# Optimization experiments

Hardware: AMD Instinct MI355X
Metric: run time of the kernel (lower is better)

## Reference

```python
import jax, jax.numpy as jnp
import numpy as np

EMA_A = 0.4      # exponential moving average decay used in Hash_ExpMovAverage
WIN = 9          # window_size
LN_EPS = 1e-3    # keras LayerNormalization default epsilon


def setup_inputs() -> dict:
    key = jax.random.key(0)
    ks = jax.random.split(key, 8)
    B, N, D, H = 8, 4096, 256, 8
    w = lambda k, shape: jax.random.normal(k, shape, jnp.float32) * 0.05
    return {
        "x": jax.random.normal(ks[0], (B, N, D), jnp.float32),
        "head_kernel": w(ks[1], (D, H, D)),
        "head_bias": w(ks[2], (H, D)),
        "down_kernel": w(ks[3], (H, D, D)),
        "down_bias": w(ks[4], (D,)),
        "value_kernel": w(ks[5], (D, D)),
        "value_bias": w(ks[6], (D,)),
        "ln_gamma": jnp.ones((D,), jnp.float32),
        "ln_beta": jnp.zeros((D,), jnp.float32),
    }


def reference(x, head_kernel, head_bias, down_kernel, down_bias,
              value_kernel, value_bias, ln_gamma, ln_beta):
    B, N, D = x.shape
    half = (WIN - 1) // 2

    # Up_Projection: [B,N,D] -> [B,N,H,D], relu
    q = jax.nn.relu(jnp.einsum('bnd,dhe->bnhe', x, head_kernel) + head_bias)

    # ---- Neighborhoods_Arrangement ----
    # Neighborhood_SimHash: sign codes from relu activations, summed over heads
    codes = 2.0 * jnp.minimum(jnp.ceil(q), 1.0) - 1.0        # [B,N,H,D]
    lsh = jnp.sum(codes, axis=-2)                            # [B,N,D]
    # Hash_ExpMovAverage: sort descending along D, add positional encoding, EMA dot
    pos = jnp.argsort(-lsh, axis=-1)                         # descending order
    lsh_sorted = jnp.take_along_axis(lsh, pos, axis=-1)
    pf = pos.astype(jnp.float32)
    freq = 10.0 ** (-(pf / jnp.float32(D)))                  # 1 / 10**powers
    pe = jnp.sin(freq) * (pf % 2) + jnp.cos(freq) * (1.0 - pf % 2)
    vals = lsh_sorted + pe / EMA_A
    c = EMA_A * (1.0 - EMA_A) ** jnp.arange(D, dtype=jnp.float32)
    simv = jnp.einsum('bnd,d->bn', vals, c)                  # [B,N]
    order = jnp.argsort(simv, axis=-1)                       # ascending
    q = jnp.take_along_axis(q, order[:, :, None, None], axis=1)  # reorder tokens

    # Down_Projection: [B,N,H,D] -> [B,N,D], relu
    q = jax.nn.relu(jnp.einsum('bnhd,hde->bne', q, down_kernel) + down_bias)

    # (matches tile-first / extract_patches / tile-last concat in the original)
    starts = jnp.clip(jnp.arange(N) - half, 0, N - WIN)      # [N]
    widx = starts[:, None] + jnp.arange(WIN)[None, :]
    keyw = q[:, widx]

    scale = jnp.sqrt(jnp.float32(D))
    scores = jax.nn.softmax(jnp.einsum('bnd,bnwd->bnw', q, keyw) / scale, axis=-1)
    value = jax.nn.relu(jnp.einsum('bnwd,de->bnwe', keyw, value_kernel) + value_bias)
    attn_out = jnp.einsum('bnwd,bnw->bnd', value, scores)

    # Residual with ORIGINAL (un-permuted) inputs + LayerNorm (keras default eps)
    y = attn_out + x
    mu = jnp.mean(y, axis=-1, keepdims=True)
    var = jnp.var(y, axis=-1, keepdims=True)
    return (y - mu) / jnp.sqrt(var + LN_EPS) * ln_gamma + ln_beta
```

## Files before the change

kernel.cpp:

```cpp
#include <hip/hip_runtime.h>

constexpr int Bc = 8, Nc = 4096;
constexpr int TN = 16;
constexpr int TN3 = 32;
constexpr int XS3 = 36;

using short8 = __attribute__((ext_vector_type(8))) short;
using f32x4  = __attribute__((ext_vector_type(4))) float;

static __device__ __forceinline__ unsigned short f2bf(float f) {
    unsigned u = __float_as_uint(f);
    u += 0x7fffu + ((u >> 16) & 1u);
    return (unsigned short)(u >> 16);
}
static __device__ __forceinline__ int swz(int r, int k) {
    return (r << 9) + ((k << 1) ^ ((r & 7) << 4));
}

__global__ __launch_bounds__(256)
void k0_wdt(const float* __restrict__ Wd, unsigned short* __restrict__ WdT)
{
    __shared__ float tile[64][65];
    const int h  = blockIdx.x >> 4;
    const int t  = blockIdx.x & 15;
    const int kb = (t >> 2) * 64, eb = (t & 3) * 64;
    const int tid = threadIdx.x;
    {
        const int krow = tid >> 2, ec = (tid & 3) * 16;
        const float* src = Wd + h * 65536 + (kb + krow) * 256 + eb + ec;
        #pragma unroll
        for (int i = 0; i < 4; ++i) {
            float4 v = *reinterpret_cast<const float4*>(src + i * 4);
            tile[krow][ec + i * 4 + 0] = v.x;
            tile[krow][ec + i * 4 + 1] = v.y;
            tile[krow][ec + i * 4 + 2] = v.z;
            tile[krow][ec + i * 4 + 3] = v.w;
        }
    }
    __syncthreads();
    {
        const int erow = tid >> 2, dc = (tid & 3) * 16;
        unsigned short o[16];
        #pragma unroll
        for (int i = 0; i < 16; ++i) o[i] = f2bf(tile[dc + i][erow]);
        unsigned short* dst = WdT + h * 65536 + (eb + erow) * 256 + kb + dc;
        *reinterpret_cast<short8*>(dst)     = *reinterpret_cast<short8*>(&o[0]);
        *reinterpret_cast<short8*>(dst + 8) = *reinterpret_cast<short8*>(&o[8]);
    }
}

__global__ __launch_bounds__(256)
void k0_wht(const float* __restrict__ Wh, unsigned short* __restrict__ WhH,
            float* __restrict__ WhT)
{
    __shared__ float tile[64][65];
    const int h  = blockIdx.x >> 4;
    const int t  = blockIdx.x & 15;
    const int kb = (t >> 2) * 64, eb = (t & 3) * 64;
    const int tid = threadIdx.x;
    {
        const int krow = tid >> 2, ec = (tid & 3) * 16;
        const float* src = Wh + (kb + krow) * 2048 + h * 256 + eb + ec;
        #pragma unroll
        for (int i = 0; i < 4; ++i) {
            float4 v = *reinterpret_cast<const float4*>(src + i * 4);
            tile[krow][ec + i * 4 + 0] = v.x;
            tile[krow][ec + i * 4 + 1] = v.y;
            tile[krow][ec + i * 4 + 2] = v.z;
            tile[krow][ec + i * 4 + 3] = v.w;
        }
    }
    __syncthreads();
    {
        const int erow = tid >> 2, dc = (tid & 3) * 16;
        unsigned short o[16];
        float of[16];
        #pragma unroll
        for (int i = 0; i < 16; ++i) {
            of[i] = tile[dc + i][erow];
            o[i] = f2bf(of[i]);
        }
        const long base = (long)h * 65536 + (eb + erow) * 256 + kb + dc;
        *reinterpret_cast<short8*>(WhH + base)     = *reinterpret_cast<short8*>(&o[0]);
        *reinterpret_cast<short8*>(WhH + base + 8) = *reinterpret_cast<short8*>(&o[8]);
        #pragma unroll
        for (int i = 0; i < 16; i += 4)
            *reinterpret_cast<float4*>(WhT + base + i) = *reinterpret_cast<const float4*>(&of[i]);
    }
}

#define XSH_OFF 0
#define QTB_OFF 8192
#define LSH_OFF 16384
#define PE_OFF  32768
#define CF_OFF  33792
#define CNT_OFF 34816
#define FCN_OFF 35840
#define FLS_OFF 35856
#define FLS_CAP 1024
#define GUARD   0.012f

__global__ __launch_bounds__(256, 2)
void k1_head_down(const float* __restrict__ x,
                  const float* __restrict__ bh,
                  const float* __restrict__ WhT,
                  const unsigned short* __restrict__ WhH,
                  const unsigned short* __restrict__ WdT, const float* __restrict__ bd,
                  float* __restrict__ z, float* __restrict__ simv)
{
    __shared__ __align__(16) char SM[40192];

    const int tid = threadIdx.x;
    const long rowbase = (long)blockIdx.x * TN;
    const int wavei = tid >> 6, lane = tid & 63;
    const int mrow = lane & 15, kgrp = lane >> 4;
    const int ebase = wavei * 64 + mrow;
    const int kfo = kgrp * 8;

    {
        const int d = tid;
        const float u = -((float)d * 0.00390625f);
        const float freq = (float)pow(10.0, (double)u);
        const float pe = (d & 1) ? (float)sin((double)freq)
                                 : (float)cos((double)freq);
        ((float*)(SM + PE_OFF))[d] = __fdiv_rn(pe, 0.4f);
        ((float*)(SM + CF_OFF))[d] = __fmul_rn(0.4f, (float)pow((double)0.6f, (double)d));
    }
    if (tid == 0) *((int*)(SM + FCN_OFF)) = 0;
    {
        const int r = tid >> 4, kc = (tid & 15) * 16;
        const float* src = x + (rowbase + r) * 256 + kc;
        unsigned short oh[16];
        #pragma unroll
        for (int i = 0; i < 16; i += 4) {
            float4 v = *reinterpret_cast<const float4*>(src + i);
            oh[i + 0] = f2bf(v.x); oh[i + 1] = f2bf(v.y);
            oh[i + 2] = f2bf(v.z); oh[i + 3] = f2bf(v.w);
        }
        *reinterpret_cast<short8*>(SM + XSH_OFF + swz(r, kc))     = *reinterpret_cast<short8*>(&oh[0]);
        *reinterpret_cast<short8*>(SM + XSH_OFF + swz(r, kc + 8)) = *reinterpret_cast<short8*>(&oh[8]);
    }

    short8 hb[3][4], db[3][4];
    #pragma unroll
    for (int nf = 0; nf < 4; ++nf) {
        hb[0][nf] = *reinterpret_cast<const short8*>(&WhH[(ebase + nf * 16) * 256 + kfo]);
        hb[1][nf] = *reinterpret_cast<const short8*>(&WhH[(ebase + nf * 16) * 256 + 32 + kfo]);
    }

    unsigned lshp0 = 0, lshp1 = 0;
    f32x4 dacc[4];
    #pragma unroll
    for (int nf = 0; nf < 4; ++nf) dacc[nf] = (f32x4){0.f, 0.f, 0.f, 0.f};

    __syncthreads();

    for (int h = 0; h < 8; ++h) {
        const unsigned short* whh = WhH + ((long)h << 16);
        const unsigned short* wdh = WdT + ((long)h << 16);
        float bias[4];
        #pragma unroll
        for (int nf = 0; nf < 4; ++nf) bias[nf] = bh[(h << 8) + ebase + nf * 16];

        f32x4 hacc[4];
        #pragma unroll
        for (int nf = 0; nf < 4; ++nf) hacc[nf] = (f32x4){0.f, 0.f, 0.f, 0.f};
        #pragma unroll
        for (int kt = 0; kt < 8; ++kt) {
            const int k0 = kt * 32 + kfo;
            short8 afh = *reinterpret_cast<const short8*>(SM + XSH_OFF + swz(mrow, k0));
            if (kt < 6) {
                #pragma unroll
                for (int nf = 0; nf < 4; ++nf)
                    hb[(kt + 2) % 3][nf] = *reinterpret_cast<const short8*>(
                        &whh[(ebase + nf * 16) * 256 + k0 + 64]);
            }
            if (kt == 6) {
                #pragma unroll
                for (int nf = 0; nf < 4; ++nf)
                    db[0][nf] = *reinterpret_cast<const short8*>(
                        &wdh[(ebase + nf * 16) * 256 + kfo]);
            }
            if (kt == 7) {
                #pragma unroll
                for (int nf = 0; nf < 4; ++nf)
                    db[1][nf] = *reinterpret_cast<const short8*>(
                        &wdh[(ebase + nf * 16) * 256 + 32 + kfo]);
            }
            #pragma unroll
            for (int nf = 0; nf < 4; ++nf)
                hacc[nf] = __builtin_amdgcn_mfma_f32_16x16x32_bf16(afh, hb[kt % 3][nf], hacc[nf], 0, 0, 0);
        }
        #pragma unroll
        for (int nf = 0; nf < 4; ++nf) {
            const int e = ebase + nf * 16;
            #pragma unroll
            for (int reg = 0; reg < 4; ++reg) {
                const int r = kgrp * 4 + reg;
                const float pre = __fadd_rn(hacc[nf][reg], bias[nf]);
                const unsigned pos = (pre > 0.0f) ? 1u : 0u;
                const int j = nf * 4 + reg;
                if (j < 8) lshp0 += pos << (4 * j); else lshp1 += pos << (4 * (j - 8));
                if (fabsf(pre) < GUARD) {
                    int idx = atomicAdd((int*)(SM + FCN_OFF), 1);
                    if (idx < FLS_CAP)
                        ((int*)(SM + FLS_OFF))[idx] =
                            r | (e << 4) | (h << 12) | ((int)pos << 15);
                }
                *reinterpret_cast<unsigned short*>(SM + QTB_OFF + swz(r, e)) =
                    f2bf(fmaxf(pre, 0.0f));
            }
        }
        __syncthreads();
        #pragma unroll
        for (int ks = 0; ks < 8; ++ks) {
            const int k0 = ks * 32 + kfo;
            short8 af = *reinterpret_cast<const short8*>(SM + QTB_OFF + swz(mrow, k0));
            if (ks < 6) {
                #pragma unroll
                for (int nf = 0; nf < 4; ++nf)
                    db[(ks + 2) % 3][nf] = *reinterpret_cast<const short8*>(
                        &wdh[(ebase + nf * 16) * 256 + k0 + 64]);
            }
            if (ks == 6 && h < 7) {
                #pragma unroll
                for (int nf = 0; nf < 4; ++nf)
                    hb[0][nf] = *reinterpret_cast<const short8*>(
                        &WhH[((long)(h + 1) << 16) + (ebase + nf * 16) * 256 + kfo]);
            }
            if (ks == 7 && h < 7) {
                #pragma unroll
                for (int nf = 0; nf < 4; ++nf)
                    hb[1][nf] = *reinterpret_cast<const short8*>(
                        &WhH[((long)(h + 1) << 16) + (ebase + nf * 16) * 256 + 32 + kfo]);
            }
            #pragma unroll
            for (int nf = 0; nf < 4; ++nf)
                dacc[nf] = __builtin_amdgcn_mfma_f32_16x16x32_bf16(af, db[ks % 3][nf], dacc[nf], 0, 0, 0);
        }
        __syncthreads();
    }
    #pragma unroll
    for (int nf = 0; nf < 4; ++nf) {
        const int e = ebase + nf * 16;
        const float b = bd[e];
        #pragma unroll
        for (int reg = 0; reg < 4; ++reg) {
            const int m = kgrp * 4 + reg;
            z[(rowbase + m) * 256 + e] = fmaxf(dacc[nf][reg] + b, 0.0f);
        }
    }
    {
        int* lshI = (int*)(SM + LSH_OFF);
        #pragma unroll
        for (int nf = 0; nf < 4; ++nf) {
            const int e = ebase + nf * 16;
            #pragma unroll
            for (int reg = 0; reg < 4; ++reg) {
                const int j = nf * 4 + reg;
                const unsigned p = ((j < 8) ? (lshp0 >> (4 * j)) : (lshp1 >> (4 * (j - 8)))) & 15u;
                lshI[e * 16 + kgrp * 4 + reg] = 2 * (int)p - 8;
            }
        }
    }
    __syncthreads();
    {
        int n = *((int*)(SM + FCN_OFF));
        n = n < FLS_CAP ? n : FLS_CAP;
        for (int i = tid; i < n; i += 256) {
            const int ent = ((int*)(SM + FLS_OFF))[i];
            const int r = ent & 15, e = (ent >> 4) & 255, hh2 = (ent >> 12) & 7;
            const int fs = ((ent >> 15) & 1) ? 1 : -1;
            const float* xr = x + (rowbase + r) * 256;
            const float* wrow = WhT + (((long)hh2 << 8) + e) * 256;
            float acc = 0.0f;
            for (int k = 0; k < 256; k += 4) {
                float4 xv = *reinterpret_cast<const float4*>(xr + k);
                float4 wv = *reinterpret_cast<const float4*>(wrow + k);
                acc = fmaf(xv.x, wv.x, acc);
                acc = fmaf(xv.y, wv.y, acc);
                acc = fmaf(xv.z, wv.z, acc);
                acc = fmaf(xv.w, wv.w, acc);
            }
            const float pre = __fadd_rn(acc, bh[hh2 * 256 + e]);
            const int es = (pre > 0.0f) ? 1 : -1;
            if (es != fs)
                atomicAdd(&((int*)(SM + LSH_OFF))[e * 16 + r], es - fs);
        }
    }
    __syncthreads();
    if (tid < TN) {
        const int r = tid;
        const int* lshI = (const int*)(SM + LSH_OFF);
        const float* pe_over = (const float*)(SM + PE_OFF);
        const float* c_f = (const float*)(SM + CF_OFF);
        int* cw = (int*)(SM + CNT_OFF) + r * 16;
        for (int i = 0; i < 9; ++i) cw[i] = 0;
        for (int d = 0; d < 256; ++d) {
            int vv = lshI[d * 16 + r];
            cw[(vv + 8) >> 1] += 1;
        }
        int run = 0;
        for (int bin = 8; bin >= 0; --bin) { int c0 = cw[bin]; cw[bin] = run; run += c0; }
        float* valq = (float*)(SM + r * 1024);
        for (int d = 0; d < 256; ++d) {
            int vv = lshI[d * 16 + r];
            int bin = (vv + 8) >> 1;
            int j = cw[bin]++;
            valq[j] = __fadd_rn((float)vv, pe_over[d]);
        }
        float L0 = 0.f, L1 = 0.f, L2 = 0.f, L3 = 0.f,
              L4 = 0.f, L5 = 0.f, L6 = 0.f, L7 = 0.f;
        for (int i = 0; i < 256; i += 8) {
            L0 = fmaf(valq[i + 0], c_f[i + 0], L0);
            L1 = fmaf(valq[i + 1], c_f[i + 1], L1);
            L2 = fmaf(valq[i + 2], c_f[i + 2], L2);
            L3 = fmaf(valq[i + 3], c_f[i + 3], L3);
            L4 = fmaf(valq[i + 4], c_f[i + 4], L4);
            L5 = fmaf(valq[i + 5], c_f[i + 5], L5);
            L6 = fmaf(valq[i + 6], c_f[i + 6], L6);
            L7 = fmaf(valq[i + 7], c_f[i + 7], L7);
        }
        const float h0 = __fadd_rn(L0, L4);
        const float h1 = __fadd_rn(L1, L5);
        const float h2 = __fadd_rn(L2, L6);
        const float h3 = __fadd_rn(L3, L7);
        simv[rowbase + r] = __fadd_rn(__fadd_rn(h0, h2), __fadd_rn(h1, h3));
    }
}

__global__ __launch_bounds__(256)
void k2_rank(const float* __restrict__ simv, int* __restrict__ order)
{
    __shared__ float s_l[4096];
    const int b = blockIdx.x >> 4;
    const int chunk = blockIdx.x & 15;
    const float* S = simv + (long)b * 4096;
    for (int i = threadIdx.x; i < 4096; i += 256) s_l[i] = S[i];
    __syncthreads();
    const int n = chunk * 256 + threadIdx.x;
    const float key = s_l[n];
    int cnt = 0;
    for (int m = 0; m < 4096; ++m) {
        float sm = s_l[m];
        cnt += (sm < key) ? 1 : ((sm == key && m < n) ? 1 : 0);
    }
    order[(long)b * 4096 + cnt] = n;
}

__global__ __launch_bounds__(256, 2)
void k3_value(const float* __restrict__ z, const int* __restrict__ order,
              const float* __restrict__ Wv, const float* __restrict__ bv,
              float* __restrict__ v)
{
    __shared__ float zT[256 * XS3];
    __shared__ int sh_ord[TN3];
    const int tid = threadIdx.x;
    const long rowbase = (long)blockIdx.x * TN3;
    const long bbase = (rowbase >> 12) << 12;
    if (tid < TN3) sh_ord[tid] = order[rowbase + tid];
    __syncthreads();
    #pragma unroll
    for (int r = 0; r < TN3; ++r)
        zT[tid * XS3 + r] = z[(bbase + sh_ord[r]) * 256 + tid];
    float acc[TN3];
    #pragma unroll
    for (int r = 0; r < TN3; ++r) acc[r] = 0.0f;
    __syncthreads();
    const float* wc = Wv + tid;
    #pragma unroll 2
    for (int k = 0; k < 256; ++k) {
        float w = wc[k * 256];
        const float* zk = &zT[k * XS3];
        #pragma unroll
        for (int r4 = 0; r4 < TN3; r4 += 4) {
            float4 zv = *reinterpret_cast<const float4*>(zk + r4);
            acc[r4 + 0] = fmaf(zv.x, w, acc[r4 + 0]);
            acc[r4 + 1] = fmaf(zv.y, w, acc[r4 + 1]);
            acc[r4 + 2] = fmaf(zv.z, w, acc[r4 + 2]);
            acc[r4 + 3] = fmaf(zv.w, w, acc[r4 + 3]);
        }
    }
    const float bias = bv[tid];
    #pragma unroll
    for (int r = 0; r < TN3; ++r)
        v[(rowbase + r) * 256 + tid] = fmaxf(acc[r] + bias, 0.0f);
}

__global__ __launch_bounds__(256)
void k4_attn_ln(const float* __restrict__ z, const float* __restrict__ v,
                const int* __restrict__ order, const float* __restrict__ x,
                const float* __restrict__ gamma, const float* __restrict__ beta,
                float* __restrict__ out)
{
    const int tid = threadIdx.x;
    const int wv = tid >> 6, lane = tid & 63;
    const long row = (long)blockIdx.x * 4 + wv;
    const int n = (int)(row & 4095);
    const long bbase = row - n;
    int start = n - 4;
    start = start < 0 ? 0 : start;
    start = start > (Nc - 9) ? (Nc - 9) : start;
    const int d0 = lane * 4;

    const int srcq = order[bbase + n];
    float4 q4 = *reinterpret_cast<const float4*>(&z[(bbase + srcq) * 256 + d0]);

    float t[9];
    #pragma unroll
    for (int w = 0; w < 9; ++w) {
        int srcm = order[bbase + start + w];
        float4 kv = *reinterpret_cast<const float4*>(&z[(bbase + srcm) * 256 + d0]);
        float p = q4.x * kv.x + q4.y * kv.y + q4.z * kv.z + q4.w * kv.w;
        #pragma unroll
        for (int off = 32; off > 0; off >>= 1) p += __shfl_xor(p, off);
        t[w] = p * 0.0625f;
    }
    float mx = t[0];
    #pragma unroll
    for (int w = 1; w < 9; ++w) mx = fmaxf(mx, t[w]);
    float pw[9], psum = 0.0f;
    #pragma unroll
    for (int w = 0; w < 9; ++w) { pw[w] = expf(t[w] - mx); psum += pw[w]; }
    const float pinv = 1.0f / psum;

    float4 a = make_float4(0.f, 0.f, 0.f, 0.f);
    #pragma unroll
    for (int w = 0; w < 9; ++w) {
        float4 vv = *reinterpret_cast<const float4*>(&v[(bbase + start + w) * 256 + d0]);
        float s = pw[w] * pinv;
        a.x = fmaf(vv.x, s, a.x);
        a.y = fmaf(vv.y, s, a.y);
        a.z = fmaf(vv.z, s, a.z);
        a.w = fmaf(vv.w, s, a.w);
    }
    float4 xv = *reinterpret_cast<const float4*>(&x[(bbase + n) * 256 + d0]);
    float4 y = make_float4(a.x + xv.x, a.y + xv.y, a.z + xv.z, a.w + xv.w);

    float s1 = y.x + y.y + y.z + y.w;
    float s2 = y.x * y.x + y.y * y.y + y.z * y.z + y.w * y.w;
    #pragma unroll
    for (int off = 32; off > 0; off >>= 1) {
        s1 += __shfl_xor(s1, off);
        s2 += __shfl_xor(s2, off);
    }
    const float mu = s1 * (1.0f / 256.0f);
    const float var = s2 * (1.0f / 256.0f) - mu * mu;
    const float istd = 1.0f / sqrtf(var + 0.001f);

    float4 g4 = *reinterpret_cast<const float4*>(&gamma[d0]);
    float4 b4 = *reinterpret_cast<const float4*>(&beta[d0]);
    float4 o;
    o.x = (y.x - mu) * istd * g4.x + b4.x;
    o.y = (y.y - mu) * istd * g4.y + b4.y;
    o.z = (y.z - mu) * istd * g4.z + b4.z;
    o.w = (y.w - mu) * istd * g4.w + b4.w;
    *reinterpret_cast<float4*>(&out[row * 256 + d0]) = o;
}

extern "C" void kernel_launch(void* const* d_in, const int* in_sizes, int n_in,
                              void* d_out, int out_size, void* d_ws, size_t ws_size,
                              hipStream_t stream)
{
    const float* x  = (const float*)d_in[0];
    const float* Wh = (const float*)d_in[1];
    const float* bh = (const float*)d_in[2];
    const float* Wd = (const float*)d_in[3];
    const float* bd = (const float*)d_in[4];
    const float* Wv = (const float*)d_in[5];
    const float* bv = (const float*)d_in[6];
    const float* g  = (const float*)d_in[7];
    const float* be = (const float*)d_in[8];
    float* out = (float*)d_out;

    char* ws = (char*)d_ws;
    float*          z     = (float*)ws;
    float*          v     = (float*)(ws + 33554432);
    float*          simv  = (float*)(ws + 67108864);
    int*            order = (int*)(ws + 67239936);
    unsigned short* WdT   = (unsigned short*)(ws + 67371008);
    unsigned short* WhH   = (unsigned short*)(ws + 68419584);
    float*          WhT   = (float*)(ws + 69468160);

    const int rows = Bc * Nc;
    k0_wdt<<<dim3(128), dim3(256), 0, stream>>>(Wd, WdT);
    k0_wht<<<dim3(128), dim3(256), 0, stream>>>(Wh, WhH, WhT);
    k1_head_down<<<dim3(rows / TN), dim3(256), 0, stream>>>(x, bh, WhT, WhH, WdT, bd, z, simv);
    k2_rank<<<dim3(Bc * 16), dim3(256), 0, stream>>>(simv, order);
    k3_value<<<dim3(rows / TN3), dim3(256), 0, stream>>>(z, order, Wv, bv, v);
    k4_attn_ln<<<dim3(rows / 4), dim3(256), 0, stream>>>(z, v, order, x, g, be, out);
}
```

Measured before the change: 916.9 us.

## Double k1 row tile to 32 and move value projection onto bf16 MFMA

The fused head/down-projection kernel now processes 32 rows per block with two M-tiles sharing each weight fragment, halving weight reloads per row. Its register weight pipeline is restructured into 4-deep buffers, and shared memory grows to about 78 KB. The value projection kernel is rewritten from scalar fp32 FMAs to bf16 MFMA, using a new pre-transposed bf16 copy of Wv. The risks are bf16 rounding in the value path and lower occupancy in k1 from the larger shared memory and register use.

```diff
diff --git a/kernel.cpp b/kernel.cpp
--- a/kernel.cpp
+++ b/kernel.cpp
@@ -1,9 +1,6 @@
 #include <hip/hip_runtime.h>
 
 constexpr int Bc = 8, Nc = 4096;
-constexpr int TN = 16;
-constexpr int TN3 = 32;
-constexpr int XS3 = 36;
 
 using short8 = __attribute__((ext_vector_type(8))) short;
 using f32x4  = __attribute__((ext_vector_type(4))) float;
@@ -89,16 +86,47 @@
     }
 }
 
-#define XSH_OFF 0
-#define QTB_OFF 8192
-#define LSH_OFF 16384
-#define PE_OFF  32768
-#define CF_OFF  33792
-#define CNT_OFF 34816
-#define FCN_OFF 35840
-#define FLS_OFF 35856
-#define FLS_CAP 1024
-#define GUARD   0.012f
+__global__ __launch_bounds__(256)
+void k0_wvt(const float* __restrict__ Wv, unsigned short* __restrict__ WvT)
+{
+    __shared__ float tile[64][65];
+    const int t  = blockIdx.x;
+    const int kb = (t >> 2) * 64, eb = (t & 3) * 64;
+    const int tid = threadIdx.x;
+    {
+        const int krow = tid >> 2, ec = (tid & 3) * 16;
+        const float* src = Wv + (kb + krow) * 256 + eb + ec;
+        #pragma unroll
+        for (int i = 0; i < 4; ++i) {
+            float4 v = *reinterpret_cast<const float4*>(src + i * 4);
+            tile[krow][ec + i * 4 + 0] = v.x;
+            tile[krow][ec + i * 4 + 1] = v.y;
+            tile[krow][ec + i * 4 + 2] = v.z;
+            tile[krow][ec + i * 4 + 3] = v.w;
+        }
+    }
+    __syncthreads();
+    {
+        const int erow = tid >> 2, dc = (tid & 3) * 16;
+        unsigned short o[16];
+        #pragma unroll
+        for (int i = 0; i < 16; ++i) o[i] = f2bf(tile[dc + i][erow]);
+        unsigned short* dst = WvT + (eb + erow) * 256 + kb + dc;
+        *reinterpret_cast<short8*>(dst)     = *reinterpret_cast<short8*>(&o[0]);
+        *reinterpret_cast<short8*>(dst + 8) = *reinterpret_cast<short8*>(&o[8]);
+    }
+}
+
+#define XSH_OFF  0
+#define QTB_OFF  16384
+#define VALQ_OFF 35072
+#define PE_OFF   67840
+#define CF_OFF   68864
+#define CNT_OFF  69888
+#define FCN_OFF  71936
+#define FLS_OFF  71952
+#define FLS_CAP  1536
+#define GUARD    0.012f
 
 __global__ __launch_bounds__(256, 2)
 void k1_head_down(const float* __restrict__ x,
@@ -108,14 +136,22 @@
                   const unsigned short* __restrict__ WdT, const float* __restrict__ bd,
                   float* __restrict__ z, float* __restrict__ simv)
 {
-    __shared__ __align__(16) char SM[40192];
+    __shared__ __align__(16) char SM[78336];
 
     const int tid = threadIdx.x;
-    const long rowbase = (long)blockIdx.x * TN;
+    const long rowbase = (long)blockIdx.x * 32;
     const int wavei = tid >> 6, lane = tid & 63;
     const int mrow = lane & 15, kgrp = lane >> 4;
     const int ebase = wavei * 64 + mrow;
     const int kfo = kgrp * 8;
+
+    short8 hB[4][4], dB[4][4];
+    #pragma unroll
+    for (int i = 0; i < 4; ++i)
+        #pragma unroll
+        for (int nf = 0; nf < 4; ++nf)
+            hB[i][nf] = *reinterpret_cast<const short8*>(
+                &WhH[(ebase + nf * 16) * 256 + i * 32 + kfo]);
 
     {
         const int d = tid;
@@ -128,30 +164,27 @@
     }
     if (tid == 0) *((int*)(SM + FCN_OFF)) = 0;
     {
-        const int r = tid >> 4, kc = (tid & 15) * 16;
+        const int r = tid >> 3, kc = (tid & 7) * 32;
         const float* src = x + (rowbase + r) * 256 + kc;
-        unsigned short oh[16];
-        #pragma unroll
-        for (int i = 0; i < 16; i += 4) {
+        unsigned short oh[32];
+        #pragma unroll
+        for (int i = 0; i < 32; i += 4) {
             float4 v = *reinterpret_cast<const float4*>(src + i);
             oh[i + 0] = f2bf(v.x); oh[i + 1] = f2bf(v.y);
             oh[i + 2] = f2bf(v.z); oh[i + 3] = f2bf(v.w);
         }
-        *reinterpret_cast<short8*>(SM + XSH_OFF + swz(r, kc))     = *reinterpret_cast<short8*>(&oh[0]);
-        *reinterpret_cast<short8*>(SM + XSH_OFF + swz(r, kc + 8)) = *reinterpret_cast<short8*>(&oh[8]);
-    }
-
-    short8 hb[3][4], db[3][4];
-    #pragma unroll
-    for (int nf = 0; nf < 4; ++nf) {
-        hb[0][nf] = *reinterpret_cast<const short8*>(&WhH[(ebase + nf * 16) * 256 + kfo]);
-        hb[1][nf] = *reinterpret_cast<const short8*>(&WhH[(ebase + nf * 16) * 256 + 32 + kfo]);
-    }
-
-    unsigned lshp0 = 0, lshp1 = 0;
-    f32x4 dacc[4];
-    #pragma unroll
-    for (int nf = 0; nf < 4; ++nf) dacc[nf] = (f32x4){0.f, 0.f, 0.f, 0.f};
+        #pragma unroll
+        for (int i = 0; i < 32; i += 8)
+            *reinterpret_cast<short8*>(SM + XSH_OFF + swz(r, kc + i)) =
+                *reinterpret_cast<short8*>(&oh[i]);
+    }
+
+    unsigned lshp[4] = {0u, 0u, 0u, 0u};
+    f32x4 dacc[2][4];
+    #pragma unroll
+    for (int mt = 0; mt < 2; ++mt)
+        #pragma unroll
+        for (int nf = 0; nf < 4; ++nf) dacc[mt][nf] = (f32x4){0.f, 0.f, 0.f, 0.f};
 
     __syncthreads();
 
@@ -162,115 +195,119 @@
         #pragma unroll
         for (int nf = 0; nf < 4; ++nf) bias[nf] = bh[(h << 8) + ebase + nf * 16];
 
-        f32x4 hacc[4];
-        #pragma unroll
-        for (int nf = 0; nf < 4; ++nf) hacc[nf] = (f32x4){0.f, 0.f, 0.f, 0.f};
+        f32x4 hacc[2][4];
+        #pragma unroll
+        for (int mt = 0; mt < 2; ++mt)
+            #pragma unroll
+            for (int nf = 0; nf < 4; ++nf) hacc[mt][nf] = (f32x4){0.f, 0.f, 0.f, 0.f};
         #pragma unroll
         for (int kt = 0; kt < 8; ++kt) {
             const int k0 = kt * 32 + kfo;
-            short8 afh = *reinterpret_cast<const short8*>(SM + XSH_OFF + swz(mrow, k0));
-            if (kt < 6) {
+            short8 a0 = *reinterpret_cast<const short8*>(SM + XSH_OFF + swz(mrow, k0));
+            short8 a1 = *reinterpret_cast<const short8*>(SM + XSH_OFF + swz(16 + mrow, k0));
+            if (kt < 4) {
                 #pragma unroll
                 for (int nf = 0; nf < 4; ++nf)
-                    hb[(kt + 2) % 3][nf] = *reinterpret_cast<const short8*>(
-                        &whh[(ebase + nf * 16) * 256 + k0 + 64]);
-            }
-            if (kt == 6) {
+                    dB[kt][nf] = *reinterpret_cast<const short8*>(
+                        &wdh[(ebase + nf * 16) * 256 + kt * 32 + kfo]);
+            }
+            #pragma unroll
+            for (int nf = 0; nf < 4; ++nf) {
+                hacc[0][nf] = __builtin_amdgcn_mfma_f32_16x16x32_bf16(a0, hB[kt & 3][nf], hacc[0][nf], 0, 0, 0);
+                hacc[1][nf] = __builtin_amdgcn_mfma_f32_16x16x32_bf16(a1, hB[kt & 3][nf], hacc[1][nf], 0, 0, 0);
+            }
+            if (kt < 4) {
                 #pragma unroll
                 for (int nf = 0; nf < 4; ++nf)
-                    db[0][nf] = *reinterpret_cast<const short8*>(
-                        &wdh[(ebase + nf * 16) * 256 + kfo]);
-            }
-            if (kt == 7) {
+                    hB[kt][nf] = *reinterpret_cast<const short8*>(
+                        &whh[(ebase + nf * 16) * 256 + (kt + 4) * 32 + kfo]);
+            }
+        }
+        #pragma unroll
+        for (int mt = 0; mt < 2; ++mt) {
+            #pragma unroll
+            for (int nf = 0; nf < 4; ++nf) {
+                const int e = ebase + nf * 16;
+                #pragma unroll
+                for (int reg = 0; reg < 4; ++reg) {
+                    const int r = mt * 16 + kgrp * 4 + reg;
+                    const float pre = __fadd_rn(hacc[mt][nf][reg], bias[nf]);
+                    const unsigned pos = (pre > 0.0f) ? 1u : 0u;
+                    const int j = mt * 16 + nf * 4 + reg;
+                    lshp[j >> 3] += pos << (4 * (j & 7));
+                    if (fabsf(pre) < GUARD) {
+                        int idx = atomicAdd((int*)(SM + FCN_OFF), 1);
+                        if (idx < FLS_CAP)
+                            ((int*)(SM + FLS_OFF))[idx] =
+                                r | (e << 5) | (h << 13) | ((int)pos << 16);
+                    }
+                    *reinterpret_cast<unsigned short*>(SM + QTB_OFF + swz(r, e)) =
+                        f2bf(fmaxf(pre, 0.0f));
+                }
+            }
+        }
+        __syncthreads();
+        #pragma unroll
+        for (int ks = 0; ks < 8; ++ks) {
+            const int k0 = ks * 32 + kfo;
+            short8 a0 = *reinterpret_cast<const short8*>(SM + QTB_OFF + swz(mrow, k0));
+            short8 a1 = *reinterpret_cast<const short8*>(SM + QTB_OFF + swz(16 + mrow, k0));
+            #pragma unroll
+            for (int nf = 0; nf < 4; ++nf) {
+                dacc[0][nf] = __builtin_amdgcn_mfma_f32_16x16x32_bf16(a0, dB[ks & 3][nf], dacc[0][nf], 0, 0, 0);
+                dacc[1][nf] = __builtin_amdgcn_mfma_f32_16x16x32_bf16(a1, dB[ks & 3][nf], dacc[1][nf], 0, 0, 0);
+            }
+            if (ks < 4) {
                 #pragma unroll
                 for (int nf = 0; nf < 4; ++nf)
-                    db[1][nf] = *reinterpret_cast<const short8*>(
-                        &wdh[(ebase + nf * 16) * 256 + 32 + kfo]);
-            }
-            #pragma unroll
-            for (int nf = 0; nf < 4; ++nf)
-                hacc[nf] = __builtin_amdgcn_mfma_f32_16x16x32_bf16(afh, hb[kt % 3][nf], hacc[nf], 0, 0, 0);
-        }
+                    dB[ks][nf] = *reinterpret_cast<const short8*>(
+                        &wdh[(ebase + nf * 16) * 256 + (ks + 4) * 32 + kfo]);
+            } else if (h < 7) {
+                #pragma unroll
+                for (int nf = 0; nf < 4; ++nf)
+                    hB[ks - 4][nf] = *reinterpret_cast<const short8*>(
+                        &WhH[((long)(h + 1) << 16) + (ebase + nf * 16) * 256 + (ks - 4) * 32 + kfo]);
+            }
+        }
+        __syncthreads();
+    }
+    #pragma unroll
+    for (int mt = 0; mt < 2; ++mt) {
         #pragma unroll
         for (int nf = 0; nf < 4; ++nf) {
             const int e = ebase + nf * 16;
-            #pragma unroll
-            for (int reg = 0; reg < 4; ++reg) {
-                const int r = kgrp * 4 + reg;
-                const float pre = __fadd_rn(hacc[nf][reg], bias[nf]);
-                const unsigned pos = (pre > 0.0f) ? 1u : 0u;
-                const int j = nf * 4 + reg;
-                if (j < 8) lshp0 += pos << (4 * j); else lshp1 += pos << (4 * (j - 8));
-                if (fabsf(pre) < GUARD) {
-                    int idx = atomicAdd((int*)(SM + FCN_OFF), 1);
-                    if (idx < FLS_CAP)
-                        ((int*)(SM + FLS_OFF))[idx] =
-                            r | (e << 4) | (h << 12) | ((int)pos << 15);
+            const float b = bd[e];
+            #pragma unroll
+            for (int reg = 0; reg < 4; ++reg)
+                z[(rowbase + mt * 16 + kgrp * 4 + reg) * 256 + e] =
+                    fmaxf(dacc[mt][nf][reg] + b, 0.0f);
+        }
+    }
+    {
+        int* lshI = (int*)SM;
+        #pragma unroll
+        for (int mt = 0; mt < 2; ++mt)
+            #pragma unroll
+            for (int nf = 0; nf < 4; ++nf) {
+                const int e = ebase + nf * 16;
+                #pragma unroll
+                for (int reg = 0; reg < 4; ++reg) {
+                    const int r = mt * 16 + kgrp * 4 + reg;
+                    const int j = mt * 16 + nf * 4 + reg;
+                    const unsigned p = (lshp[j >> 3] >> (4 * (j & 7))) & 15u;
+                    lshI[e * 34 + r] = 2 * (int)p - 8;
                 }
-                *reinterpret_cast<unsigned short*>(SM + QTB_OFF + swz(r, e)) =
-                    f2bf(fmaxf(pre, 0.0f));
-            }
-        }
-        __syncthreads();
-        #pragma unroll
-        for (int ks = 0; ks < 8; ++ks) {
-            const int k0 = ks * 32 + kfo;
-            short8 af = *reinterpret_cast<const short8*>(SM + QTB_OFF + swz(mrow, k0));
-            if (ks < 6) {
-                #pragma unroll
-                for (int nf = 0; nf < 4; ++nf)
-                    db[(ks + 2) % 3][nf] = *reinterpret_cast<const short8*>(
-                        &wdh[(ebase + nf * 16) * 256 + k0 + 64]);
-            }
-            if (ks == 6 && h < 7) {
-                #pragma unroll
-                for (int nf = 0; nf < 4; ++nf)
-                    hb[0][nf] = *reinterpret_cast<const short8*>(
-                        &WhH[((long)(h + 1) << 16) + (ebase + nf * 16) * 256 + kfo]);
-            }
-            if (ks == 7 && h < 7) {
-                #pragma unroll
-                for (int nf = 0; nf < 4; ++nf)
-                    hb[1][nf] = *reinterpret_cast<const short8*>(
-                        &WhH[((long)(h + 1) << 16) + (ebase + nf * 16) * 256 + 32 + kfo]);
-            }
-            #pragma unroll
-            for (int nf = 0; nf < 4; ++nf)
-                dacc[nf] = __builtin_amdgcn_mfma_f32_16x16x32_bf16(af, db[ks % 3][nf], dacc[nf], 0, 0, 0);
-        }
-        __syncthreads();
-    }
-    #pragma unroll
-    for (int nf = 0; nf < 4; ++nf) {
-        const int e = ebase + nf * 16;
-        const float b = bd[e];
-        #pragma unroll
-        for (int reg = 0; reg < 4; ++reg) {
-            const int m = kgrp * 4 + reg;
-            z[(rowbase + m) * 256 + e] = fmaxf(dacc[nf][reg] + b, 0.0f);
-        }
-    }
-    {
-        int* lshI = (int*)(SM + LSH_OFF);
-        #pragma unroll
-        for (int nf = 0; nf < 4; ++nf) {
-            const int e = ebase + nf * 16;
-            #pragma unroll
-            for (int reg = 0; reg < 4; ++reg) {
-                const int j = nf * 4 + reg;
-                const unsigned p = ((j < 8) ? (lshp0 >> (4 * j)) : (lshp1 >> (4 * (j - 8)))) & 15u;
-                lshI[e * 16 + kgrp * 4 + reg] = 2 * (int)p - 8;
-            }
-        }
-    }
-    __syncthreads();
-    {
+            }
+    }
+    __syncthreads();
+    {
+        int* lshI = (int*)SM;
         int n = *((int*)(SM + FCN_OFF));
         n = n < FLS_CAP ? n : FLS_CAP;
         for (int i = tid; i < n; i += 256) {
             const int ent = ((int*)(SM + FLS_OFF))[i];
-            const int r = ent & 15, e = (ent >> 4) & 255, hh2 = (ent >> 12) & 7;
-            const int fs = ((ent >> 15) & 1) ? 1 : -1;
+            const int r = ent & 31, e = (ent >> 5) & 255, hh2 = (ent >> 13) & 7;
+            const int fs = ((ent >> 16) & 1) ? 1 : -1;
             const float* xr = x + (rowbase + r) * 256;
             const float* wrow = WhT + (((long)hh2 << 8) + e) * 256;
             float acc = 0.0f;
@@ -285,26 +322,26 @@
             const float pre = __fadd_rn(acc, bh[hh2 * 256 + e]);
             const int es = (pre > 0.0f) ? 1 : -1;
             if (es != fs)
-                atomicAdd(&((int*)(SM + LSH_OFF))[e * 16 + r], es - fs);
-        }
-    }
-    __syncthreads();
-    if (tid < TN) {
+                atomicAdd(&lshI[e * 34 + r], es - fs);
+        }
+    }
+    __syncthreads();
+    if (tid < 32) {
         const int r = tid;
-        const int* lshI = (const int*)(SM + LSH_OFF);
+        const int* lshI = (const int*)SM;
         const float* pe_over = (const float*)(SM + PE_OFF);
         const float* c_f = (const float*)(SM + CF_OFF);
         int* cw = (int*)(SM + CNT_OFF) + r * 16;
         for (int i = 0; i < 9; ++i) cw[i] = 0;
         for (int d = 0; d < 256; ++d) {
-            int vv = lshI[d * 16 + r];
+            int vv = lshI[d * 34 + r];
             cw[(vv + 8) >> 1] += 1;
         }
         int run = 0;
         for (int bin = 8; bin >= 0; --bin) { int c0 = cw[bin]; cw[bin] = run; run += c0; }
-        float* valq = (float*)(SM + r * 1024);
+        float* valq = (float*)(SM + VALQ_OFF + r * 1024);
         for (int d = 0; d < 256; ++d) {
-            int vv = lshI[d * 16 + r];
+            int vv = lshI[d * 34 + r];
             int bin = (vv + 8) >> 1;
             int j = cw[bin]++;
             valq[j] = __fadd_rn((float)vv, pe_over[d]);
@@ -348,43 +385,83 @@
     order[(long)b * 4096 + cnt] = n;
 }
 
-__global__ __launch_bounds__(256, 2)
+__global__ __launch_bounds__(256, 3)
 void k3_value(const float* __restrict__ z, const int* __restrict__ order,
-              const float* __restrict__ Wv, const float* __restrict__ bv,
+              const unsigned short* __restrict__ WvT, const float* __restrict__ bv,
               float* __restrict__ v)
 {
-    __shared__ float zT[256 * XS3];
-    __shared__ int sh_ord[TN3];
+    __shared__ __align__(16) unsigned short ZB[32 * 256];
+    __shared__ int ord[32];
     const int tid = threadIdx.x;
-    const long rowbase = (long)blockIdx.x * TN3;
+    const long rowbase = (long)blockIdx.x * 32;
     const long bbase = (rowbase >> 12) << 12;
-    if (tid < TN3) sh_ord[tid] = order[rowbase + tid];
-    __syncthreads();
-    #pragma unroll
-    for (int r = 0; r < TN3; ++r)
-        zT[tid * XS3 + r] = z[(bbase + sh_ord[r]) * 256 + tid];
-    float acc[TN3];
-    #pragma unroll
-    for (int r = 0; r < TN3; ++r) acc[r] = 0.0f;
-    __syncthreads();
-    const float* wc = Wv + tid;
-    #pragma unroll 2
-    for (int k = 0; k < 256; ++k) {
-        float w = wc[k * 256];
-        const float* zk = &zT[k * XS3];
-        #pragma unroll
-        for (int r4 = 0; r4 < TN3; r4 += 4) {
-            float4 zv = *reinterpret_cast<const float4*>(zk + r4);
-            acc[r4 + 0] = fmaf(zv.x, w, acc[r4 + 0]);
-            acc[r4 + 1] = fmaf(zv.y, w, acc[r4 + 1]);
-            acc[r4 + 2] = fmaf(zv.z, w, acc[r4 + 2]);
-            acc[r4 + 3] = fmaf(zv.w, w, acc[r4 + 3]);
-        }
-    }
-    const float bias = bv[tid];
-    #pragma unroll
-    for (int r = 0; r < TN3; ++r)
-        v[(rowbase + r) * 256 + tid] = fmaxf(acc[r] + bias, 0.0f);
+    const int wavei = tid >> 6, lane = tid & 63;
+    const int mrow = lane & 15, kgrp = lane >> 4;
+    const int ebase = wavei * 64 + mrow;
+    const int kfo = kgrp * 8;
+
+    if (tid < 32) ord[tid] = order[rowbase + tid];
+
+    short8 vB[4][4];
+    #pragma unroll
+    for (int i = 0; i < 4; ++i)
+        #pragma unroll
+        for (int nf = 0; nf < 4; ++nf)
+            vB[i][nf] = *reinterpret_cast<const short8*>(
+                &WvT[(ebase + nf * 16) * 256 + i * 32 + kfo]);
+
+    __syncthreads();
+    {
+        const int r = tid >> 3, kc = (tid & 7) * 32;
+        const float* src = z + (bbase + ord[r]) * 256 + kc;
+        unsigned short oh[32];
+        #pragma unroll
+        for (int i = 0; i < 32; i += 4) {
+            float4 vv = *reinterpret_cast<const float4*>(src + i);
+            oh[i + 0] = f2bf(vv.x); oh[i + 1] = f2bf(vv.y);
+            oh[i + 2] = f2bf(vv.z); oh[i + 3] = f2bf(vv.w);
+        }
+        #pragma unroll
+        for (int i = 0; i < 32; i += 8)
+            *reinterpret_cast<short8*>((char*)ZB + swz(r, kc + i)) =
+                *reinterpret_cast<short8*>(&oh[i]);
+    }
+    __syncthreads();
+
+    f32x4 acc[2][4];
+    #pragma unroll
+    for (int mt = 0; mt < 2; ++mt)
+        #pragma unroll
+        for (int nf = 0; nf < 4; ++nf) acc[mt][nf] = (f32x4){0.f, 0.f, 0.f, 0.f};
+    #pragma unroll
+    for (int kt = 0; kt < 8; ++kt) {
+        const int k0 = kt * 32 + kfo;
+        short8 a0 = *reinterpret_cast<const short8*>((char*)ZB + swz(mrow, k0));
+        short8 a1 = *reinterpret_cast<const short8*>((char*)ZB + swz(16 + mrow, k0));
+        #pragma unroll
+        for (int nf = 0; nf < 4; ++nf) {
+            acc[0][nf] = __builtin_amdgcn_mfma_f32_16x16x32_bf16(a0, vB[kt & 3][nf], acc[0][nf], 0, 0, 0);
+            acc[1][nf] = __builtin_amdgcn_mfma_f32_16x16x32_bf16(a1, vB[kt & 3][nf], acc[1][nf], 0, 0, 0);
+        }
+        if (kt < 4) {
+            #pragma unroll
+            for (int nf = 0; nf < 4; ++nf)
+                vB[kt][nf] = *reinterpret_cast<const short8*>(
+                    &WvT[(ebase + nf * 16) * 256 + (kt + 4) * 32 + kfo]);
+        }
+    }
+    #pragma unroll
+    for (int mt = 0; mt < 2; ++mt) {
+        #pragma unroll
+        for (int nf = 0; nf < 4; ++nf) {
+            const int e = ebase + nf * 16;
+            const float b = bv[e];
+            #pragma unroll
+            for (int reg = 0; reg < 4; ++reg)
+                v[(rowbase + mt * 16 + kgrp * 4 + reg) * 256 + e] =
+                    fmaxf(acc[mt][nf][reg] + b, 0.0f);
+        }
+    }
 }
 
 __global__ __launch_bounds__(256)
@@ -481,12 +558,14 @@
     unsigned short* WdT   = (unsigned short*)(ws + 67371008);
     unsigned short* WhH   = (unsigned short*)(ws + 68419584);
     float*          WhT   = (float*)(ws + 69468160);
+    unsigned short* WvT   = (unsigned short*)(ws + 71565312);
 
     const int rows = Bc * Nc;
     k0_wdt<<<dim3(128), dim3(256), 0, stream>>>(Wd, WdT);
     k0_wht<<<dim3(128), dim3(256), 0, stream>>>(Wh, WhH, WhT);
-    k1_head_down<<<dim3(rows / TN), dim3(256), 0, stream>>>(x, bh, WhT, WhH, WdT, bd, z, simv);
+    k0_wvt<<<dim3(16), dim3(256), 0, stream>>>(Wv, WvT);
+    k1_head_down<<<dim3(rows / 32), dim3(256), 0, stream>>>(x, bh, WhT, WhH, WdT, bd, z, simv);
     k2_rank<<<dim3(Bc * 16), dim3(256), 0, stream>>>(simv, order);
-    k3_value<<<dim3(rows / TN3), dim3(256), 0, stream>>>(z, order, Wv, bv, v);
+    k3_value<<<dim3(rows / 32), dim3(256), 0, stream>>>(z, order, WvT, bv, v);
     k4_attn_ln<<<dim3(rows / 4), dim3(256), 0, stream>>>(z, v, order, x, g, be, out);
 }
```

Measured after the change: 744.2 us. 18.8% less time.
